# Kernel optimization log

Measured on AMD Instinct MI355X. Metric: run time of the kernel, lower is better.

Reference implementation:

```python
import jax, jax.numpy as jnp
import numpy as np

B, IN_DIM, EXP_DIM, E = 16384, 256, 128, 8  # batch, input_dim, expert_dim, expert_num


def setup_inputs() -> dict:
    key = jax.random.key(0)
    ks = jax.random.split(key, 12)
    s_in = 1.0 / np.sqrt(IN_DIM)
    return {
        "x_a": jax.random.normal(ks[0], (B, IN_DIM), jnp.float32),
        "x_b": jax.random.normal(ks[1], (B, IN_DIM), jnp.float32),
        "x_share": jax.random.normal(ks[2], (B, IN_DIM), jnp.float32),
        # expert banks: [E, IN_DIM, EXP_DIM] weights, [E, EXP_DIM] bias
        "Wa": jax.random.uniform(ks[3], (E, IN_DIM, EXP_DIM), jnp.float32, -s_in, s_in),
        "ba": jax.random.uniform(ks[4], (E, EXP_DIM), jnp.float32, -s_in, s_in),
        "Wb": jax.random.uniform(ks[5], (E, IN_DIM, EXP_DIM), jnp.float32, -s_in, s_in),
        "bb": jax.random.uniform(ks[6], (E, EXP_DIM), jnp.float32, -s_in, s_in),
        "Ws": jax.random.uniform(ks[7], (E, IN_DIM, EXP_DIM), jnp.float32, -s_in, s_in),
        "bs": jax.random.uniform(ks[8], (E, EXP_DIM), jnp.float32, -s_in, s_in),
        # gate projections (bias=False): num single-output linears == one [num, IN_DIM] matrix
        "Ga": jax.random.uniform(ks[9], (2 * E, IN_DIM), jnp.float32, -s_in, s_in),
        "Gb": jax.random.uniform(ks[10], (2 * E, IN_DIM), jnp.float32, -s_in, s_in),
        "Gs": jax.random.uniform(ks[11], (3 * E, IN_DIM), jnp.float32, -s_in, s_in),
    }


def _experts(x, W, b):
    # batched dense stack: [B,IN] x [E,IN,D] -> [B,E,D]
    return jnp.einsum("bi,eid->bed", x, W) + b[None, :, :]


def _gate(x, G, experts):
    # logits [B, num]; softmax over experts; weighted sum over expert axis
    w = jax.nn.softmax(x @ G.T, axis=1)
    return jnp.einsum("be,bed->bd", w, experts)


def reference(x_a, x_b, x_share, Wa, ba, Wb, bb, Ws, bs, Ga, Gb, Gs):
    ea = _experts(x_a, Wa, ba)          # [B,E,D]
    eb = _experts(x_b, Wb, bb)          # [B,E,D]
    es = _experts(x_share, Ws, bs)      # [B,E,D]
    out_a = _gate(x_a, Ga, jnp.concatenate([ea, es], axis=1))
    out_b = _gate(x_b, Gb, jnp.concatenate([eb, es], axis=1))
    out_s = _gate(x_share, Gs, jnp.concatenate([ea, eb, es], axis=1))
    return (out_a, out_b, out_s)
```

## Files before the change

### kernel.cpp

```cpp
#include <hip/hip_runtime.h>
#include <stdint.h>

#define BATCH 16384
#define INDIM 256
#define DDIM  128
#define NEXP  8
#define ROWS  64
#define THREADS 512
#define NSEQ  96
#define QSLB  4096

typedef __bf16 bfv8  __attribute__((ext_vector_type(8)));
typedef float  f32x4 __attribute__((ext_vector_type(4)));

typedef __attribute__((address_space(1))) const void gas_void;
typedef __attribute__((address_space(3))) void las_void;

__global__ void prep_kernel(const float* __restrict__ Wa, const float* __restrict__ Wb,
                            const float* __restrict__ Ws, const float* __restrict__ Ga,
                            const float* __restrict__ Gb, const float* __restrict__ Gs,
                            __bf16* __restrict__ wp, __bf16* __restrict__ gp) {
    __shared__ float ws[32 * 132];
    const int b = blockIdx.x, tid = threadIdx.x;
    if (b < 192) {
        const int st = b >> 6, e = (b >> 3) & 7, kt = b & 7;
        const float* W = (st == 0) ? Wa : (st == 1) ? Wb : Ws;
        const float* src = W + (size_t)(e * 256 + kt * 32) * 128;
#pragma unroll
        for (int k = 0; k < 4; k++) {
            int idx4 = tid + k * 256;
            f32x4 v = *(const f32x4*)(src + (size_t)idx4 * 4);
            int row = idx4 >> 5;
            int col = (idx4 & 31) << 2;
            ws[row * 132 + col + 0] = v[0];
            ws[row * 132 + col + 1] = v[1];
            ws[row * 132 + col + 2] = v[2];
            ws[row * 132 + col + 3] = v[3];
        }
        __syncthreads();
        __bf16* o = wp + ((size_t)b << 12);
#pragma unroll
        for (int h2 = 0; h2 < 2; h2++) {
            int base = tid * 2 + h2;
            int nt = base >> 6, lane = base & 63;
            int d  = nt * 16 + (lane & 15);
            int i0 = (lane >> 4) * 8;
            bfv8 ov;
#pragma unroll
            for (int j = 0; j < 8; j++) ov[j] = (__bf16)ws[(i0 + j) * 132 + d];
            *(bfv8*)(o + (size_t)base * 8) = ov;
        }
    } else {
        int t2 = (b - 192) * 256 + tid;
        int lane = t2 & 63, nt = (t2 >> 6) & 3, kt = t2 >> 8;
        int g  = nt * 16 + (lane & 15);
        int k0 = kt * 32 + (lane >> 4) * 8;
        __bf16* o = gp + (size_t)t2 * 8;
#pragma unroll
        for (int j = 0; j < 8; j++) {
            int k = k0 + j;
            float v = 0.f;
            if (g < 16)      v = Ga[g * 256 + k];
            else if (g < 32) v = Gb[(g - 16) * 256 + k];
            else if (g < 56) v = Gs[(g - 32) * 256 + k];
            o[j] = (__bf16)v;
        }
    }
}

__device__ __forceinline__ void load_afr(const float* __restrict__ x, int rb,
                                         int l16, int quad, bfv8 afr[2][8]) {
#pragma unroll
    for (int mt = 0; mt < 2; mt++) {
        const float* xr = x + (size_t)(rb + mt * 16 + l16) * INDIM;
#pragma unroll
        for (int kt = 0; kt < 8; kt++) {
            const f32x4* p = (const f32x4*)(xr + kt * 32 + quad * 8);
            f32x4 lo = __builtin_nontemporal_load(p);
            f32x4 hi = __builtin_nontemporal_load(p + 1);
            bfv8 a;
            a[0] = (__bf16)lo[0]; a[1] = (__bf16)lo[1]; a[2] = (__bf16)lo[2]; a[3] = (__bf16)lo[3];
            a[4] = (__bf16)hi[0]; a[5] = (__bf16)hi[1]; a[6] = (__bf16)hi[2]; a[7] = (__bf16)hi[3];
            afr[mt][kt] = a;
        }
    }
}

__device__ __forceinline__ void load_afr16(const float* __restrict__ x, int rbase,
                                           int l16, int quad, bfv8 afr[8]) {
    const float* xr = x + (size_t)(rbase + l16) * INDIM;
#pragma unroll
    for (int kt = 0; kt < 8; kt++) {
        const f32x4* p = (const f32x4*)(xr + kt * 32 + quad * 8);
        f32x4 lo = __builtin_nontemporal_load(p);
        f32x4 hi = __builtin_nontemporal_load(p + 1);
        bfv8 a;
        a[0] = (__bf16)lo[0]; a[1] = (__bf16)lo[1]; a[2] = (__bf16)lo[2]; a[3] = (__bf16)lo[3];
        a[4] = (__bf16)hi[0]; a[5] = (__bf16)hi[1]; a[6] = (__bf16)hi[2]; a[7] = (__bf16)hi[3];
        afr[kt] = a;
    }
}

__device__ __forceinline__ void stage_kt2(const __bf16* __restrict__ wp,
                                          __bf16* ring, int ks, int slot,
                                          int co, int wv, int lane) {
    const __bf16* src = wp + ((size_t)(ks + (wv >> 2)) << 12)
                           + (co << 11) + ((wv & 3) << 9) + (lane << 3);
    __bf16* dst = ring + (slot << 12) + ((size_t)wv << 9);
    __builtin_amdgcn_global_load_lds((gas_void*)src, (las_void*)dst, 16, 0, 0);
}

__device__ __forceinline__ int ks_of(int s, int rot) {
    int st = s >> 5;
    int eb = (((s >> 2) & 7) + rot) & 7;
    return st * 64 + eb * 8 + (s & 3) * 2;
}

__launch_bounds__(THREADS, 2)
__global__ void ple_kernel(const float* __restrict__ xa, const float* __restrict__ xb,
                           const float* __restrict__ xs,
                           const float* __restrict__ ba, const float* __restrict__ bb,
                           const float* __restrict__ bs,
                           const __bf16* __restrict__ wp, const __bf16* __restrict__ gp,
                           float* __restrict__ out) {
    __shared__ __bf16 ring[2 * QSLB];
    __shared__ float lgt[ROWS * 64];
    __shared__ float wT[64 * ROWS];

    const int tid  = threadIdx.x;
    const int wv   = tid >> 6;
    const int lane = tid & 63;
    const int quad = lane >> 4;
    const int l16  = lane & 15;
    const int bid  = blockIdx.x;
    const int r0   = (bid >> 1) * ROWS;
    const int co   = bid & 1;
    const int rot  = (bid >> 3) & 7;

    stage_kt2(wp, ring, ks_of(0, rot), 0, co, wv, lane);

    {
        const int rg = wv >> 2;
        const int cg = wv & 3;
        const int rb = r0 + rg * 32;
        bfv8 afr[2][8];
        const float* x = (cg == 0) ? xa : (cg == 1) ? xb : xs;
        load_afr(x, rb, l16, quad, afr);
        f32x4 acc1[2];
#pragma unroll
        for (int mt = 0; mt < 2; mt++) { f32x4 z = {0.f, 0.f, 0.f, 0.f}; acc1[mt] = z; }
#pragma unroll
        for (int kt = 0; kt < 8; kt++) {
            bfv8 gfr = *(const bfv8*)(gp + ((size_t)(kt * 4 + cg) * 64 + lane) * 8);
#pragma unroll
            for (int mt = 0; mt < 2; mt++)
                acc1[mt] = __builtin_amdgcn_mfma_f32_16x16x32_bf16(afr[mt][kt], gfr, acc1[mt], 0, 0, 0);
        }
#pragma unroll
        for (int mt = 0; mt < 2; mt++)
#pragma unroll
            for (int r = 0; r < 4; r++)
                lgt[(rg * 32 + mt * 16 + quad * 4 + r) * 64 + cg * 16 + l16] = acc1[mt][r];
    }
    __syncthreads();

    if (tid < ROWS) {
        const float* L = lgt + tid * 64;
#pragma unroll
        for (int gi = 0; gi < 3; gi++) {
            const int base = (gi == 0) ? 0 : (gi == 1 ? 16 : 32);
            const int cnt  = (gi == 2) ? 24 : 16;
            float m = -1e30f;
            for (int k = 0; k < cnt; k++) m = fmaxf(m, L[base + k]);
            float s = 0.f;
            for (int k = 0; k < cnt; k++) s += __expf(L[base + k] - m);
            float inv = 1.f / s;
            for (int k = 0; k < cnt; k++) wT[(base + k) * ROWS + tid] = __expf(L[base + k] - m) * inv;
        }
    }
    __syncthreads();

    const int rg2   = wv >> 1;
    const int cgl   = wv & 1;
    const int rbase = r0 + rg2 * 16;

    bfv8 afr2[8];
    float o[3][2][4];
#pragma unroll
    for (int oi = 0; oi < 3; oi++)
#pragma unroll
        for (int ntl = 0; ntl < 2; ntl++)
#pragma unroll
            for (int r = 0; r < 4; r++) o[oi][ntl][r] = 0.f;

#define FOLD(oi, gbase)                                                              \
    {                                                                                \
        f32x4 gw4 = *(const f32x4*)(wT + (gbase + eb) * ROWS + rg2 * 16 + quad * 4); \
        _Pragma("unroll")                                                            \
        for (int ntl = 0; ntl < 2; ntl++)                                            \
            _Pragma("unroll")                                                        \
            for (int r = 0; r < 4; r++)                                              \
                o[oi][ntl][r] += gw4[r] * acc[ntl][r];                               \
    }

#pragma unroll
    for (int st = 0; st < 3; st++) {
        const float* x    = (st == 0) ? xa : (st == 1) ? xb : xs;
        const float* bias = (st == 0) ? ba : (st == 1) ? bb : bs;
        load_afr16(x, rbase, l16, quad, afr2);

#pragma unroll 1
        for (int eb0 = 0; eb0 < NEXP; eb0++) {
            const int eb = (eb0 + rot) & 7;
            float b0 = bias[eb * 128 + co * 64 + cgl * 32 + l16];
            float b1 = bias[eb * 128 + co * 64 + cgl * 32 + 16 + l16];

            f32x4 acc[2];
#pragma unroll
            for (int ntl = 0; ntl < 2; ntl++) { f32x4 z = {0.f, 0.f, 0.f, 0.f}; acc[ntl] = z; }

#pragma unroll
            for (int q = 0; q < 4; q++) {
                const int s = st * 32 + eb0 * 4 + q;
                __syncthreads();
                if (s + 1 < NSEQ)
                    stage_kt2(wp, ring, ks_of(s + 1, rot), (s + 1) & 1, co, wv, lane);

                const __bf16* buf = ring + ((s & 1) << 12);
#pragma unroll
                for (int j = 0; j < 2; j++) {
                    const int kt = q * 2 + j;
                    const __bf16* reg = buf + (j << 11) + (cgl << 10);
                    bfv8 bv0 = *(const bfv8*)(reg + ((size_t)lane << 3));
                    bfv8 bv1 = *(const bfv8*)(reg + 512 + ((size_t)lane << 3));
                    acc[0] = __builtin_amdgcn_mfma_f32_16x16x32_bf16(afr2[kt], bv0, acc[0], 0, 0, 0);
                    acc[1] = __builtin_amdgcn_mfma_f32_16x16x32_bf16(afr2[kt], bv1, acc[1], 0, 0, 0);
                }
            }

#pragma unroll
            for (int r = 0; r < 4; r++) { acc[0][r] += b0; acc[1][r] += b1; }

            if (st == 0)      { FOLD(0, 0);  FOLD(2, 32); }
            else if (st == 1) { FOLD(1, 16); FOLD(2, 40); }
            else              { FOLD(0, 8);  FOLD(1, 24); FOLD(2, 48); }
        }
    }
#undef FOLD

#pragma unroll
    for (int oi = 0; oi < 3; oi++) {
        float* ob = out + (size_t)oi * BATCH * DDIM;
#pragma unroll
        for (int r = 0; r < 4; r++) {
            int row = rbase + quad * 4 + r;
#pragma unroll
            for (int ntl = 0; ntl < 2; ntl++)
                __builtin_nontemporal_store(o[oi][ntl][r],
                    &ob[(size_t)row * DDIM + co * 64 + cgl * 32 + ntl * 16 + l16]);
        }
    }
}

extern "C" void kernel_launch(void* const* d_in, const int* in_sizes, int n_in,
                              void* d_out, int out_size, void* d_ws, size_t ws_size,
                              hipStream_t stream) {
    const float* xa = (const float*)d_in[0];
    const float* xb = (const float*)d_in[1];
    const float* xs = (const float*)d_in[2];
    const float* Wa = (const float*)d_in[3];
    const float* ba = (const float*)d_in[4];
    const float* Wb = (const float*)d_in[5];
    const float* bb = (const float*)d_in[6];
    const float* Ws = (const float*)d_in[7];
    const float* bs = (const float*)d_in[8];
    const float* Ga = (const float*)d_in[9];
    const float* Gb = (const float*)d_in[10];
    const float* Gs = (const float*)d_in[11];

    __bf16* wp = (__bf16*)d_ws;
    __bf16* gp = wp + 3 * 8 * 8 * 8 * 64 * 8;

    prep_kernel<<<200, 256, 0, stream>>>(Wa, Wb, Ws, Ga, Gb, Gs, wp, gp);
    ple_kernel<<<2 * (BATCH / ROWS), THREADS, 0, stream>>>(xa, xb, xs, ba, bb, bs, wp, gp, (float*)d_out);
}
```

Measured before the change: 195.8 us.

## Double rows per block and register-block two M tiles per wave

ROWS grows from 64 to 128. Each wave now holds A fragments for 32 rows (two 16-row M tiles) and reuses every LDS-staged expert weight fragment across both tiles. The gate-logit pass loops twice to cover the larger tile. The aim is to halve the weight staging and LDS reads per output row, at the cost of more VGPRs for fragments and accumulators, a larger LDS footprint for logits and weights, and half as many blocks (256), which reduces parallelism across the CUs.

Result: no change. 194.7 us (-0.6%).

```diff
diff --git a/kernel.cpp b/kernel.cpp
--- a/kernel.cpp
+++ b/kernel.cpp
@@ -5,7 +5,7 @@
 #define INDIM 256
 #define DDIM  128
 #define NEXP  8
-#define ROWS  64
+#define ROWS  128
 #define THREADS 512
 #define NSEQ  96
 #define QSLB  4096
@@ -86,21 +86,6 @@
     }
 }
 
-__device__ __forceinline__ void load_afr16(const float* __restrict__ x, int rbase,
-                                           int l16, int quad, bfv8 afr[8]) {
-    const float* xr = x + (size_t)(rbase + l16) * INDIM;
-#pragma unroll
-    for (int kt = 0; kt < 8; kt++) {
-        const f32x4* p = (const f32x4*)(xr + kt * 32 + quad * 8);
-        f32x4 lo = __builtin_nontemporal_load(p);
-        f32x4 hi = __builtin_nontemporal_load(p + 1);
-        bfv8 a;
-        a[0] = (__bf16)lo[0]; a[1] = (__bf16)lo[1]; a[2] = (__bf16)lo[2]; a[3] = (__bf16)lo[3];
-        a[4] = (__bf16)hi[0]; a[5] = (__bf16)hi[1]; a[6] = (__bf16)hi[2]; a[7] = (__bf16)hi[3];
-        afr[kt] = a;
-    }
-}
-
 __device__ __forceinline__ void stage_kt2(const __bf16* __restrict__ wp,
                                           __bf16* ring, int ks, int slot,
                                           int co, int wv, int lane) {
@@ -142,25 +127,28 @@
     {
         const int rg = wv >> 2;
         const int cg = wv & 3;
-        const int rb = r0 + rg * 32;
+        const float* x = (cg == 0) ? xa : (cg == 1) ? xb : xs;
         bfv8 afr[2][8];
-        const float* x = (cg == 0) ? xa : (cg == 1) ? xb : xs;
-        load_afr(x, rb, l16, quad, afr);
-        f32x4 acc1[2];
-#pragma unroll
-        for (int mt = 0; mt < 2; mt++) { f32x4 z = {0.f, 0.f, 0.f, 0.f}; acc1[mt] = z; }
-#pragma unroll
-        for (int kt = 0; kt < 8; kt++) {
-            bfv8 gfr = *(const bfv8*)(gp + ((size_t)(kt * 4 + cg) * 64 + lane) * 8);
+#pragma unroll
+        for (int pass = 0; pass < 2; pass++) {
+            const int rb = r0 + pass * 64 + rg * 32;
+            load_afr(x, rb, l16, quad, afr);
+            f32x4 acc1[2];
+#pragma unroll
+            for (int mt = 0; mt < 2; mt++) { f32x4 z = {0.f, 0.f, 0.f, 0.f}; acc1[mt] = z; }
+#pragma unroll
+            for (int kt = 0; kt < 8; kt++) {
+                bfv8 gfr = *(const bfv8*)(gp + ((size_t)(kt * 4 + cg) * 64 + lane) * 8);
+#pragma unroll
+                for (int mt = 0; mt < 2; mt++)
+                    acc1[mt] = __builtin_amdgcn_mfma_f32_16x16x32_bf16(afr[mt][kt], gfr, acc1[mt], 0, 0, 0);
+            }
 #pragma unroll
             for (int mt = 0; mt < 2; mt++)
-                acc1[mt] = __builtin_amdgcn_mfma_f32_16x16x32_bf16(afr[mt][kt], gfr, acc1[mt], 0, 0, 0);
-        }
-#pragma unroll
-        for (int mt = 0; mt < 2; mt++)
-#pragma unroll
-            for (int r = 0; r < 4; r++)
-                lgt[(rg * 32 + mt * 16 + quad * 4 + r) * 64 + cg * 16 + l16] = acc1[mt][r];
+#pragma unroll
+                for (int r = 0; r < 4; r++)
+                    lgt[(pass * 64 + rg * 32 + mt * 16 + quad * 4 + r) * 64 + cg * 16 + l16] = acc1[mt][r];
+        }
     }
     __syncthreads();
 
@@ -182,32 +170,37 @@
 
     const int rg2   = wv >> 1;
     const int cgl   = wv & 1;
-    const int rbase = r0 + rg2 * 16;
-
-    bfv8 afr2[8];
-    float o[3][2][4];
+    const int rbase = r0 + rg2 * 32;
+
+    bfv8 afr2[2][8];
+    float o[3][2][2][4];
 #pragma unroll
     for (int oi = 0; oi < 3; oi++)
 #pragma unroll
-        for (int ntl = 0; ntl < 2; ntl++)
-#pragma unroll
-            for (int r = 0; r < 4; r++) o[oi][ntl][r] = 0.f;
-
-#define FOLD(oi, gbase)                                                              \
-    {                                                                                \
-        f32x4 gw4 = *(const f32x4*)(wT + (gbase + eb) * ROWS + rg2 * 16 + quad * 4); \
-        _Pragma("unroll")                                                            \
-        for (int ntl = 0; ntl < 2; ntl++)                                            \
-            _Pragma("unroll")                                                        \
-            for (int r = 0; r < 4; r++)                                              \
-                o[oi][ntl][r] += gw4[r] * acc[ntl][r];                               \
+        for (int mt = 0; mt < 2; mt++)
+#pragma unroll
+            for (int ntl = 0; ntl < 2; ntl++)
+#pragma unroll
+                for (int r = 0; r < 4; r++) o[oi][mt][ntl][r] = 0.f;
+
+#define FOLD(oi, gbase)                                                                 \
+    {                                                                                   \
+        _Pragma("unroll")                                                               \
+        for (int mt = 0; mt < 2; mt++) {                                                \
+            f32x4 gw4 = *(const f32x4*)(wT + (gbase + eb) * ROWS + rg2 * 32 + mt * 16 + quad * 4); \
+            _Pragma("unroll")                                                           \
+            for (int ntl = 0; ntl < 2; ntl++)                                           \
+                _Pragma("unroll")                                                       \
+                for (int r = 0; r < 4; r++)                                             \
+                    o[oi][mt][ntl][r] += gw4[r] * acc[mt][ntl][r];                      \
+        }                                                                               \
     }
 
 #pragma unroll
     for (int st = 0; st < 3; st++) {
         const float* x    = (st == 0) ? xa : (st == 1) ? xb : xs;
         const float* bias = (st == 0) ? ba : (st == 1) ? bb : bs;
-        load_afr16(x, rbase, l16, quad, afr2);
+        load_afr(x, rbase, l16, quad, afr2);
 
 #pragma unroll 1
         for (int eb0 = 0; eb0 < NEXP; eb0++) {
@@ -215,9 +208,11 @@
             float b0 = bias[eb * 128 + co * 64 + cgl * 32 + l16];
             float b1 = bias[eb * 128 + co * 64 + cgl * 32 + 16 + l16];
 
-            f32x4 acc[2];
-#pragma unroll
-            for (int ntl = 0; ntl < 2; ntl++) { f32x4 z = {0.f, 0.f, 0.f, 0.f}; acc[ntl] = z; }
+            f32x4 acc[2][2];
+#pragma unroll
+            for (int mt = 0; mt < 2; mt++)
+#pragma unroll
+                for (int ntl = 0; ntl < 2; ntl++) { f32x4 z = {0.f, 0.f, 0.f, 0.f}; acc[mt][ntl] = z; }
 
 #pragma unroll
             for (int q = 0; q < 4; q++) {
@@ -233,13 +228,17 @@
                     const __bf16* reg = buf + (j << 11) + (cgl << 10);
                     bfv8 bv0 = *(const bfv8*)(reg + ((size_t)lane << 3));
                     bfv8 bv1 = *(const bfv8*)(reg + 512 + ((size_t)lane << 3));
-                    acc[0] = __builtin_amdgcn_mfma_f32_16x16x32_bf16(afr2[kt], bv0, acc[0], 0, 0, 0);
-                    acc[1] = __builtin_amdgcn_mfma_f32_16x16x32_bf16(afr2[kt], bv1, acc[1], 0, 0, 0);
+                    acc[0][0] = __builtin_amdgcn_mfma_f32_16x16x32_bf16(afr2[0][kt], bv0, acc[0][0], 0, 0, 0);
+                    acc[1][0] = __builtin_amdgcn_mfma_f32_16x16x32_bf16(afr2[1][kt], bv0, acc[1][0], 0, 0, 0);
+                    acc[0][1] = __builtin_amdgcn_mfma_f32_16x16x32_bf16(afr2[0][kt], bv1, acc[0][1], 0, 0, 0);
+                    acc[1][1] = __builtin_amdgcn_mfma_f32_16x16x32_bf16(afr2[1][kt], bv1, acc[1][1], 0, 0, 0);
                 }
             }
 
 #pragma unroll
-            for (int r = 0; r < 4; r++) { acc[0][r] += b0; acc[1][r] += b1; }
+            for (int mt = 0; mt < 2; mt++)
+#pragma unroll
+                for (int r = 0; r < 4; r++) { acc[mt][0][r] += b0; acc[mt][1][r] += b1; }
 
             if (st == 0)      { FOLD(0, 0);  FOLD(2, 32); }
             else if (st == 1) { FOLD(1, 16); FOLD(2, 40); }
@@ -252,13 +251,15 @@
     for (int oi = 0; oi < 3; oi++) {
         float* ob = out + (size_t)oi * BATCH * DDIM;
 #pragma unroll
-        for (int r = 0; r < 4; r++) {
-            int row = rbase + quad * 4 + r;
-#pragma unroll
-            for (int ntl = 0; ntl < 2; ntl++)
-                __builtin_nontemporal_store(o[oi][ntl][r],
-                    &ob[(size_t)row * DDIM + co * 64 + cgl * 32 + ntl * 16 + l16]);
-        }
+        for (int mt = 0; mt < 2; mt++)
+#pragma unroll
+            for (int r = 0; r < 4; r++) {
+                int row = rbase + mt * 16 + quad * 4 + r;
+#pragma unroll
+                for (int ntl = 0; ntl < 2; ntl++)
+                    __builtin_nontemporal_store(o[oi][mt][ntl][r],
+                        &ob[(size_t)row * DDIM + co * 64 + cgl * 32 + ntl * 16 + l16]);
+            }
     }
 }
 
```
